# Kernel optimization log

Measured on AMD Instinct MI355X. Metric: run time of the kernel, lower is better.

Reference implementation:

```python
import jax, jax.numpy as jnp
import numpy as np

N = 50000
E = 800000
F0, F1, F2 = 256, 128, 64
EPS = 1e-5


def setup_inputs() -> dict:
    key = jax.random.key(0)
    ks = jax.random.split(key, 20)
    x = jax.random.normal(ks[0], (N, F0), dtype=jnp.float32)
    src = jax.random.randint(ks[1], (E,), 0, N)
    dst = jax.random.randint(ks[2], (E,), 0, N)
    edge_index = jnp.stack([src, dst]).astype(jnp.int64)

    def lin(k, fi, fo):
        s = 1.0 / np.sqrt(fi)
        k1, k2 = jax.random.split(k)
        W = jax.random.uniform(k1, (fi, fo), minval=-s, maxval=s, dtype=jnp.float32)
        b = jax.random.uniform(k2, (fo,), minval=-s, maxval=s, dtype=jnp.float32)
        return W, b

    We1, be1 = lin(ks[3], F0, F1)
    We2, be2 = lin(ks[4], F1, F2)
    Wd1, bd1 = lin(ks[5], F2, F1)
    Wd2, bd2 = lin(ks[6], F1, F0)
    return {
        'x': x, 'edge_index': edge_index,
        'We1': We1, 'be1': be1, 'g1': jnp.ones((F1,)), 'bb1': jnp.zeros((F1,)),
        'We2': We2, 'be2': be2, 'g2': jnp.ones((F2,)), 'bb2': jnp.zeros((F2,)),
        'Wd1': Wd1, 'bd1': bd1, 'g3': jnp.ones((F1,)), 'bb3': jnp.zeros((F1,)),
        'Wd2': Wd2, 'bd2': bd2, 'g4': jnp.ones((F0,)), 'bb4': jnp.zeros((F0,)),
    }


def _gcn(x, W, b, src, dst, dinv_src_dst, dinv_self):
    # PyG GCNConv: linear first, then sym-normalized propagation with self-loops
    h = x @ W + b                               # [N, Fout]
    msg = h[src] * dinv_src_dst[:, None]        # [E, Fout]
    out = jax.ops.segment_sum(msg, dst, num_segments=N)
    return out + h * dinv_self[:, None]         # self-loop term


def _bn(x, g, b):
    # BatchNorm1d training-mode: biased batch stats over node dim
    m = jnp.mean(x, axis=0)
    v = jnp.mean(jnp.square(x - m), axis=0)
    return g * (x - m) * jax.lax.rsqrt(v + EPS) + b


def reference(x, edge_index, We1, be1, g1, bb1, We2, be2, g2, bb2,
              Wd1, bd1, g3, bb3, Wd2, bd2, g4, bb4):
    src, dst = edge_index[0], edge_index[1]
    deg = jnp.zeros((N,), x.dtype).at[dst].add(1.0) + 1.0  # in-degree + self-loop
    dinv = jax.lax.rsqrt(deg)
    dsd = dinv[src] * dinv[dst]
    dself = dinv * dinv

    relu = jax.nn.relu
    # Encoder block 0 (outer i==0): relu(GCN), relu(BN)
    h = relu(_gcn(x, We1, be1, src, dst, dsd, dself))
    h = relu(_bn(h, g1, bb1))
    enc1 = h
    # Encoder block 1 (outer i==1 == len(inner)-1): relu(GCN), BN (no relu)
    h = relu(_gcn(h, We2, be2, src, dst, dsd, dself))
    h = _bn(h, g2, bb2)
    enc2 = h
    # Decoder block 0: relu(GCN), relu(BN)
    h = relu(_gcn(h, Wd1, bd1, src, dst, dsd, dself))
    h = relu(_bn(h, g3, bb3))
    # Decoder block 1 (i==1): relu(GCN), BN (no relu)
    h = relu(_gcn(h, Wd2, bd2, src, dst, dsd, dself))
    h = _bn(h, g4, bb4)
    # AE returns (reconstruction, encoded_embeddings)
    return h, enc1, enc2
```

## Files before the change

### kernel.cpp

```cpp
#include <hip/hip_runtime.h>
#include <hip/hip_fp16.h>

#define N_NODES 50000
#define F0 256
#define F1 128
#define F2 64
#define BN_EPS 1e-5f

typedef float f32x4 __attribute__((ext_vector_type(4)));
typedef __bf16 bf16x8 __attribute__((ext_vector_type(8)));
typedef unsigned short ushort8v __attribute__((ext_vector_type(8)));

__device__ __forceinline__ float bflo(unsigned v) { return __uint_as_float(v << 16); }
__device__ __forceinline__ float bfhi(unsigned v) { return __uint_as_float(v & 0xFFFF0000u); }
__device__ __forceinline__ unsigned short f2bf(float f) {
  unsigned u = __float_as_uint(f);
  u += 0x7FFFu + ((u >> 16) & 1u);
  return (unsigned short)(u >> 16);
}
__device__ __forceinline__ void split2(float a, unsigned short& hi, unsigned short& lo) {
  hi = f2bf(a);
  float hf = __uint_as_float((unsigned)hi << 16);
  lo = f2bf(a - hf);
}
__device__ __forceinline__ int rdl(int v, int l) { return __builtin_amdgcn_readlane(v, l); }
__device__ __forceinline__ float h2f(unsigned short h) {
  __half hh = *reinterpret_cast<__half*>(&h);
  return __half2float(hh);
}
__device__ __forceinline__ unsigned short f2h(float f) {
  __half hh = __float2half(f);
  return *reinterpret_cast<unsigned short*>(&hh);
}

__global__ void count_dst(const int* __restrict__ dst, int* __restrict__ counts,
                          int* __restrict__ eslot, int E) {
  int e = blockIdx.x * blockDim.x + threadIdx.x;
  if (e < E) eslot[e] = atomicAdd(&counts[dst[e]], 1);
}

__global__ __launch_bounds__(256) void scan_blocks(const int* __restrict__ counts,
                                                   int* __restrict__ offs,
                                                   int* __restrict__ bsum,
                                                   float* __restrict__ dinv) {
  __shared__ int s_w[4];
  const int tid = threadIdx.x, lane = tid & 63, wid = tid >> 6;
  const int base = blockIdx.x * 1024 + tid * 4;
  int v0 = 0, v1 = 0, v2 = 0, v3 = 0;
  if (base + 3 < N_NODES) {
    int4 v = *(const int4*)(counts + base);
    v0 = v.x; v1 = v.y; v2 = v.z; v3 = v.w;
  } else if (base < N_NODES) {
    v0 = counts[base];
    if (base + 1 < N_NODES) v1 = counts[base + 1];
    if (base + 2 < N_NODES) v2 = counts[base + 2];
  }
  if (base < N_NODES) {
    dinv[base] = rsqrtf((float)v0 + 1.0f);
    if (base + 1 < N_NODES) dinv[base + 1] = rsqrtf((float)v1 + 1.0f);
    if (base + 2 < N_NODES) dinv[base + 2] = rsqrtf((float)v2 + 1.0f);
    if (base + 3 < N_NODES) dinv[base + 3] = rsqrtf((float)v3 + 1.0f);
  }
  int t = v0 + v1 + v2 + v3;
  int incl = t;
#pragma unroll
  for (int d = 1; d < 64; d <<= 1) {
    int x = __shfl_up(incl, d);
    if (lane >= d) incl += x;
  }
  if (lane == 63) s_w[wid] = incl;
  __syncthreads();
  int woff = 0;
#pragma unroll
  for (int j = 0; j < 4; j++)
    if (j < wid) woff += s_w[j];
  int p = woff + incl - t;
  if (base < N_NODES) offs[base] = p;
  p += v0;
  if (base + 1 < N_NODES) offs[base + 1] = p;
  p += v1;
  if (base + 2 < N_NODES) offs[base + 2] = p;
  p += v2;
  if (base + 3 < N_NODES) offs[base + 3] = p;
  if (tid == 255) bsum[blockIdx.x] = woff + incl;
}

__global__ void scan_tops(int* __restrict__ bsum, int* __restrict__ offs, int nblk) {
  int lane = threadIdx.x;
  int v = (lane < nblk) ? bsum[lane] : 0;
  int incl = v;
#pragma unroll
  for (int d = 1; d < 64; d <<= 1) {
    int x = __shfl_up(incl, d);
    if (lane >= d) incl += x;
  }
  if (lane < nblk) bsum[lane] = incl - v;
  if (lane == 63) offs[N_NODES] = incl;
}

__global__ __launch_bounds__(256) void scan_add(int* __restrict__ offs,
                                                const int* __restrict__ bsum) {
  const int add = bsum[blockIdx.x];
  const int base = blockIdx.x * 1024 + threadIdx.x * 4;
  if (base + 3 < N_NODES) {
    int4 v = *(const int4*)(offs + base);
    v.x += add; v.y += add; v.z += add; v.w += add;
    *(int4*)(offs + base) = v;
  } else if (base < N_NODES) {
    offs[base] += add;
    if (base + 1 < N_NODES) offs[base + 1] += add;
    if (base + 2 < N_NODES) offs[base + 2] += add;
  }
}

__global__ void fill_csr(const int* __restrict__ src, const int* __restrict__ dst,
                         const int* __restrict__ offs, const int* __restrict__ eslot,
                         const float* __restrict__ dinv,
                         unsigned* __restrict__ csrU, int E) {
  int e = blockIdx.x * blockDim.x + threadIdx.x;
  if (e < E) {
    int s = src[e], d = dst[e];
    int p = offs[d] + eslot[e];
    unsigned ent = (unsigned)s | ((unsigned)f2h(dinv[s]) << 16);
    __builtin_nontemporal_store(ent, &csrU[p]);
  }
}

__global__ void compute_rowsum(const int* __restrict__ offs,
                               const unsigned* __restrict__ csrU,
                               const float* __restrict__ dinv, float* __restrict__ rowsum) {
  int i = blockIdx.x * blockDim.x + threadIdx.x;
  if (i < N_NODES) {
    float di = dinv[i];
    float s = di;
    int e1 = offs[i + 1];
    for (int e = offs[i]; e < e1; e++) s += h2f((unsigned short)(csrU[e] >> 16));
    rowsum[i] = di * s;
  }
}

__device__ __forceinline__ void wt_one(const float* W, unsigned short* Wh, unsigned short* Wl,
                                       int K, int N, int idx) {
  int k = idx / N, n = idx - k * N;
  unsigned short h, l;
  split2(W[idx], h, l);
  Wh[(size_t)n * K + k] = h;
  Wl[(size_t)n * K + k] = l;
}

__global__ void convert_weights(const float* __restrict__ We1, const float* __restrict__ We2,
                                const float* __restrict__ Wd1, const float* __restrict__ Wd2,
                                unsigned short* W1h, unsigned short* W1l,
                                unsigned short* W2h, unsigned short* W2l,
                                unsigned short* W3h, unsigned short* W3l,
                                unsigned short* W4h, unsigned short* W4l) {
  int idx = blockIdx.x * blockDim.x + threadIdx.x;
  if (idx < 32768) {
    wt_one(We1, W1h, W1l, 256, 128, idx);
  } else if (idx < 40960) {
    wt_one(We2, W2h, W2l, 128, 64, idx - 32768);
  } else if (idx < 49152) {
    wt_one(Wd1, W3h, W3l, 64, 128, idx - 40960);
  } else if (idx < 81920) {
    wt_one(Wd2, W4h, W4l, 128, 256, idx - 49152);
  }
}

template <int BN, bool STATS, bool AF32>
__global__ __launch_bounds__(256) void mfma_gemm_split(
    const unsigned short* __restrict__ Ahi, const unsigned short* __restrict__ Alo,
    const float* __restrict__ Af,
    const unsigned short* __restrict__ Whi, const unsigned short* __restrict__ Wlo,
    const float* __restrict__ bias, const float* __restrict__ rowsum,
    unsigned short* __restrict__ Cb, float* __restrict__ Cf,
    float* __restrict__ stat, int M, int K, int N) {
  constexpr int BM = 128;
  constexpr int MT = (BN == 128) ? 4 : 2;
  constexpr int NT = 4;
  __shared__ __align__(16) unsigned short AsH[4][BM][8];
  __shared__ __align__(16) unsigned short AsL[4][BM][8];
  __shared__ __align__(16) unsigned short BsH[4][BN][8];
  __shared__ __align__(16) unsigned short BsL[4][BN][8];
  const int tid = threadIdx.x;
  const int lane = tid & 63, wid = tid >> 6;
  const int quad = lane >> 4, ln = lane & 15;
  const int m0 = blockIdx.x * BM;
  const int n0 = blockIdx.y * BN;
  const int wm = (BN == 128) ? (wid & 1) * 64 : wid * 32;
  const int wn = (BN == 128) ? (wid >> 1) * 64 : 0;
  f32x4 acc[MT][NT] = {};

  const int arow = tid >> 2, aseg = tid & 3;
  for (int k0 = 0; k0 < K; k0 += 32) {
#pragma unroll
    for (int i = 0; i < 2; i++) {
      int row = arow + i * 64;
      int gm = m0 + row;
      if (AF32) {
        float4 u0 = make_float4(0.f, 0.f, 0.f, 0.f), u1 = u0;
        if (gm < M) {
          u0 = *(const float4*)(Af + (size_t)gm * K + k0 + aseg * 8);
          u1 = *(const float4*)(Af + (size_t)gm * K + k0 + aseg * 8 + 4);
        }
        ushort4 h0, l0, h1, l1;
        split2(u0.x, h0.x, l0.x); split2(u0.y, h0.y, l0.y);
        split2(u0.z, h0.z, l0.z); split2(u0.w, h0.w, l0.w);
        split2(u1.x, h1.x, l1.x); split2(u1.y, h1.y, l1.y);
        split2(u1.z, h1.z, l1.z); split2(u1.w, h1.w, l1.w);
        *(ushort4*)(&AsH[aseg][row][0]) = h0;
        *(ushort4*)(&AsH[aseg][row][4]) = h1;
        *(ushort4*)(&AsL[aseg][row][0]) = l0;
        *(ushort4*)(&AsL[aseg][row][4]) = l1;
      } else {
        ushort8v vh = {0, 0, 0, 0, 0, 0, 0, 0};
        ushort8v vl = {0, 0, 0, 0, 0, 0, 0, 0};
        if (gm < M) {
          vh = *(const ushort8v*)(Ahi + (size_t)gm * K + k0 + aseg * 8);
          vl = *(const ushort8v*)(Alo + (size_t)gm * K + k0 + aseg * 8);
        }
        *(ushort8v*)(&AsH[aseg][row][0]) = vh;
        *(ushort8v*)(&AsL[aseg][row][0]) = vl;
      }
    }
#pragma unroll
    for (int i = 0; i < BN / 64; i++) {
      int n = arow + i * 64;
      *(ushort8v*)(&BsH[aseg][n][0]) =
          *(const ushort8v*)(Whi + (size_t)(n0 + n) * K + k0 + aseg * 8);
      *(ushort8v*)(&BsL[aseg][n][0]) =
          *(const ushort8v*)(Wlo + (size_t)(n0 + n) * K + k0 + aseg * 8);
    }
    __syncthreads();
    bf16x8 ah[MT], al[MT], bh[NT], bl[NT];
#pragma unroll
    for (int mt = 0; mt < MT; mt++) {
      ah[mt] = *(const bf16x8*)(&AsH[quad][wm + mt * 16 + ln][0]);
      al[mt] = *(const bf16x8*)(&AsL[quad][wm + mt * 16 + ln][0]);
    }
#pragma unroll
    for (int nt = 0; nt < NT; nt++) {
      bh[nt] = *(const bf16x8*)(&BsH[quad][wn + nt * 16 + ln][0]);
      bl[nt] = *(const bf16x8*)(&BsL[quad][wn + nt * 16 + ln][0]);
    }
#pragma unroll
    for (int mt = 0; mt < MT; mt++)
#pragma unroll
      for (int nt = 0; nt < NT; nt++) {
        acc[mt][nt] = __builtin_amdgcn_mfma_f32_16x16x32_bf16(ah[mt], bl[nt], acc[mt][nt], 0, 0, 0);
        acc[mt][nt] = __builtin_amdgcn_mfma_f32_16x16x32_bf16(al[mt], bh[nt], acc[mt][nt], 0, 0, 0);
        acc[mt][nt] = __builtin_amdgcn_mfma_f32_16x16x32_bf16(ah[mt], bh[nt], acc[mt][nt], 0, 0, 0);
      }
    __syncthreads();
  }

  if (!STATS) {
#pragma unroll
    for (int nt = 0; nt < NT; nt++) {
      int gn = n0 + wn + nt * 16 + ln;
      float bv = bias[gn];
#pragma unroll
      for (int mt = 0; mt < MT; mt++) {
#pragma unroll
        for (int r = 0; r < 4; r++) {
          int gm = m0 + wm + mt * 16 + quad * 4 + r;
          if (gm < M) Cb[(size_t)gm * N + gn] = f2bf(acc[mt][nt][r] + bv);
        }
      }
    }
  } else {
    float rs[MT][4];
#pragma unroll
    for (int mt = 0; mt < MT; mt++)
#pragma unroll
      for (int r = 0; r < 4; r++) {
        int gm = m0 + wm + mt * 16 + quad * 4 + r;
        rs[mt][r] = (gm < M) ? rowsum[gm] : 0.f;
      }
#pragma unroll
    for (int nt = 0; nt < NT; nt++) {
      int gn = n0 + wn + nt * 16 + ln;
      float bv = bias[gn];
      float ls = 0.f, lq = 0.f;
#pragma unroll
      for (int mt = 0; mt < MT; mt++) {
#pragma unroll
        for (int r = 0; r < 4; r++) {
          int gm = m0 + wm + mt * 16 + quad * 4 + r;
          if (gm < M) {
            float v = fmaxf(fmaf(bv, rs[mt][r], acc[mt][nt][r]), 0.f);
            Cf[(size_t)gm * N + gn] = v;
            ls += v;
            lq = fmaf(v, v, lq);
          }
        }
      }
      ls += __shfl_xor(ls, 16); ls += __shfl_xor(ls, 32);
      lq += __shfl_xor(lq, 16); lq += __shfl_xor(lq, 32);
      if (quad == 0) {
        atomicAdd(&stat[gn], ls);
        atomicAdd(&stat[256 + gn], lq);
      }
    }
  }
}

template <bool RELU_STATS, bool OUT_SPLIT>
__global__ __launch_bounds__(256) void agg128_rl(
    const unsigned short* __restrict__ hb, const int* __restrict__ offs,
    const unsigned* __restrict__ csrU, const float* __restrict__ dinv,
    float* __restrict__ outf, unsigned short* __restrict__ outhi,
    unsigned short* __restrict__ outlo, float* __restrict__ stat) {
  const int tid = threadIdx.x;
  const int lane = tid & 63;
  const int widx = tid >> 6;
  const int nwaves = gridDim.x * 4;
  float ls0 = 0.f, ls1 = 0.f, lq0 = 0.f, lq1 = 0.f;

  for (int node = blockIdx.x * 4 + widx; node < N_NODES; node += nwaves) {
    const int e0 = __builtin_amdgcn_readfirstlane(offs[node]);
    const int e1 = __builtin_amdgcn_readfirstlane(offs[node + 1]);
    float a0 = 0.f, a1 = 0.f;
    for (int e = e0; e < e1; e += 64) {
      const int cnt = min(64, e1 - e);
      unsigned ent = 0;
      if (lane < cnt) ent = csrU[e + lane];
      const int nb = (cnt + 7) & ~7;
      for (int j = 0; j < nb; j += 8) {
#pragma unroll
        for (int u = 0; u < 8; u++) {
          unsigned ce = (unsigned)rdl((int)ent, j + u);
          int s = (int)(ce & 0xFFFFu);
          float w = h2f((unsigned short)(ce >> 16));
          unsigned v = *(const unsigned*)(hb + (size_t)s * 128 + lane * 2);
          a0 = fmaf(bflo(v), w, a0);
          a1 = fmaf(bfhi(v), w, a1);
        }
      }
    }
    float di = dinv[node];
    unsigned vs = *(const unsigned*)(hb + (size_t)node * 128 + lane * 2);
    a0 = fmaf(bflo(vs), di, a0) * di;
    a1 = fmaf(bfhi(vs), di, a1) * di;
    if (RELU_STATS) {
      a0 = fmaxf(a0, 0.f);
      a1 = fmaxf(a1, 0.f);
      ls0 += a0; ls1 += a1;
      lq0 = fmaf(a0, a0, lq0);
      lq1 = fmaf(a1, a1, lq1);
    }
    if (OUT_SPLIT) {
      unsigned short h0, l0, h1, l1;
      split2(a0, h0, l0);
      split2(a1, h1, l1);
      *(unsigned*)(outhi + (size_t)node * 128 + lane * 2) = (unsigned)h0 | ((unsigned)h1 << 16);
      *(unsigned*)(outlo + (size_t)node * 128 + lane * 2) = (unsigned)l0 | ((unsigned)l1 << 16);
    } else {
      *(float2*)(outf + (size_t)node * 128 + lane * 2) = make_float2(a0, a1);
    }
  }

  if (RELU_STATS) {
    __shared__ float red[4][128];
    red[widx][lane * 2 + 0] = ls0;
    red[widx][lane * 2 + 1] = ls1;
    __syncthreads();
    if (tid < 128) {
      atomicAdd(&stat[tid], red[0][tid] + red[1][tid] + red[2][tid] + red[3][tid]);
    }
    __syncthreads();
    red[widx][lane * 2 + 0] = lq0;
    red[widx][lane * 2 + 1] = lq1;
    __syncthreads();
    if (tid < 128) {
      atomicAdd(&stat[256 + tid], red[0][tid] + red[1][tid] + red[2][tid] + red[3][tid]);
    }
  }
}

template <bool RELU_STATS, bool OUT_SPLIT>
__global__ __launch_bounds__(256) void agg64_rl(
    const unsigned short* __restrict__ hb, const int* __restrict__ offs,
    const unsigned* __restrict__ csrU, const float* __restrict__ dinv,
    float* __restrict__ outf, unsigned short* __restrict__ outhi,
    unsigned short* __restrict__ outlo, float* __restrict__ stat) {
  const int tid = threadIdx.x;
  const int lane = tid & 63;
  const int widx = tid >> 6;
  const int half = lane >> 5;
  const int hl = lane & 31;
  const int nwaves = gridDim.x * 4;
  float ls0 = 0.f, ls1 = 0.f, lq0 = 0.f, lq1 = 0.f;

  for (int node = blockIdx.x * 4 + widx; node < N_NODES; node += nwaves) {
    const int e0 = __builtin_amdgcn_readfirstlane(offs[node]);
    const int e1 = __builtin_amdgcn_readfirstlane(offs[node + 1]);
    float a0 = 0.f, a1 = 0.f;
    for (int e = e0; e < e1; e += 64) {
      const int cnt = min(64, e1 - e);
      unsigned ent = 0;
      if (lane < cnt) ent = csrU[e + lane];
      const int nb = (cnt + 15) & ~15;
      for (int j = 0; j < nb; j += 16) {
#pragma unroll
        for (int u = 0; u < 8; u++) {
          unsigned ca = (unsigned)rdl((int)ent, j + 2 * u);
          unsigned cb = (unsigned)rdl((int)ent, j + 2 * u + 1);
          unsigned ce = half ? cb : ca;
          int s = (int)(ce & 0xFFFFu);
          float w = h2f((unsigned short)(ce >> 16));
          unsigned v = *(const unsigned*)(hb + (size_t)s * 64 + hl * 2);
          a0 = fmaf(bflo(v), w, a0);
          a1 = fmaf(bfhi(v), w, a1);
        }
      }
    }
    a0 += __shfl_xor(a0, 32);
    a1 += __shfl_xor(a1, 32);
    float di = dinv[node];
    unsigned vs = *(const unsigned*)(hb + (size_t)node * 64 + hl * 2);
    a0 = fmaf(bflo(vs), di, a0) * di;
    a1 = fmaf(bfhi(vs), di, a1) * di;
    if (RELU_STATS) {
      a0 = fmaxf(a0, 0.f);
      a1 = fmaxf(a1, 0.f);
      if (half == 0) {
        ls0 += a0; ls1 += a1;
        lq0 = fmaf(a0, a0, lq0);
        lq1 = fmaf(a1, a1, lq1);
      }
    }
    if (half == 0) {
      if (OUT_SPLIT) {
        unsigned short h0, l0, h1, l1;
        split2(a0, h0, l0);
        split2(a1, h1, l1);
        *(unsigned*)(outhi + (size_t)node * 64 + hl * 2) = (unsigned)h0 | ((unsigned)h1 << 16);
        *(unsigned*)(outlo + (size_t)node * 64 + hl * 2) = (unsigned)l0 | ((unsigned)l1 << 16);
      } else {
        *(float2*)(outf + (size_t)node * 64 + hl * 2) = make_float2(a0, a1);
      }
    }
  }

  if (RELU_STATS) {
    __shared__ float red[4][64];
    if (half == 0) {
      red[widx][hl * 2 + 0] = ls0;
      red[widx][hl * 2 + 1] = ls1;
    }
    __syncthreads();
    if (tid < 64) {
      atomicAdd(&stat[tid], red[0][tid] + red[1][tid] + red[2][tid] + red[3][tid]);
    }
    __syncthreads();
    if (half == 0) {
      red[widx][hl * 2 + 0] = lq0;
      red[widx][hl * 2 + 1] = lq1;
    }
    __syncthreads();
    if (tid < 64) {
      atomicAdd(&stat[256 + tid], red[0][tid] + red[1][tid] + red[2][tid] + red[3][tid]);
    }
  }
}

template <int F, bool RELU, bool WF32, bool WB16, bool WSPLIT>
__global__ __launch_bounds__(256) void bn_apply_f(const float* __restrict__ a,
                                                  const float* __restrict__ stat,
                                                  const float* __restrict__ g,
                                                  const float* __restrict__ bb,
                                                  float* __restrict__ outf,
                                                  unsigned short* __restrict__ outb,
                                                  unsigned short* __restrict__ outhi,
                                                  unsigned short* __restrict__ outlo) {
  __shared__ float s_scale[F], s_shift[F];
  const int tid = threadIdx.x;
  if (tid < F) {
    const float invN = 1.0f / (float)N_NODES;
    float mean = stat[tid] * invN;
    float var = fmaxf(stat[256 + tid] * invN - mean * mean, 0.f);
    float inv = rsqrtf(var + BN_EPS);
    float sc = g[tid] * inv;
    s_scale[tid] = sc;
    s_shift[tid] = bb[tid] - mean * sc;
  }
  __syncthreads();
  constexpr int C4 = F / 4;
  const int total = N_NODES * C4;
  for (int idx = blockIdx.x * blockDim.x + tid; idx < total; idx += gridDim.x * blockDim.x) {
    int c4 = idx % C4;
    float4 v = ((const float4*)a)[idx];
    float4 s = *(float4*)&s_scale[c4 * 4];
    float4 sh = *(float4*)&s_shift[c4 * 4];
    float4 o;
    o.x = fmaf(v.x, s.x, sh.x);
    o.y = fmaf(v.y, s.y, sh.y);
    o.z = fmaf(v.z, s.z, sh.z);
    o.w = fmaf(v.w, s.w, sh.w);
    if (RELU) {
      o.x = fmaxf(o.x, 0.f);
      o.y = fmaxf(o.y, 0.f);
      o.z = fmaxf(o.z, 0.f);
      o.w = fmaxf(o.w, 0.f);
    }
    if (WF32) ((float4*)outf)[idx] = o;
    if (WB16) {
      ushort4 b;
      b.x = f2bf(o.x); b.y = f2bf(o.y); b.z = f2bf(o.z); b.w = f2bf(o.w);
      ((ushort4*)outb)[idx] = b;
    }
    if (WSPLIT) {
      ushort4 h, l;
      split2(o.x, h.x, l.x);
      split2(o.y, h.y, l.y);
      split2(o.z, h.z, l.z);
      split2(o.w, h.w, l.w);
      ((ushort4*)outhi)[idx] = h;
      ((ushort4*)outlo)[idx] = l;
    }
  }
}

extern "C" void kernel_launch(void* const* d_in, const int* in_sizes, int n_in,
                              void* d_out, int out_size, void* d_ws, size_t ws_size,
                              hipStream_t stream) {
  const float* x = (const float*)d_in[0];
  const int* ei = (const int*)d_in[1];
  const int E = in_sizes[1] / 2;
  const int* src = ei;
  const int* dst = ei + E;
  const float* We1 = (const float*)d_in[2];  const float* be1 = (const float*)d_in[3];
  const float* g1  = (const float*)d_in[4];  const float* bb1 = (const float*)d_in[5];
  const float* We2 = (const float*)d_in[6];  const float* be2 = (const float*)d_in[7];
  const float* g2  = (const float*)d_in[8];  const float* bb2 = (const float*)d_in[9];
  const float* Wd1 = (const float*)d_in[10]; const float* bd1 = (const float*)d_in[11];
  const float* g3  = (const float*)d_in[12]; const float* bb3 = (const float*)d_in[13];
  const float* Wd2 = (const float*)d_in[14]; const float* bd2 = (const float*)d_in[15];
  const float* g4  = (const float*)d_in[16]; const float* bb4 = (const float*)d_in[17];

  float* out = (float*)d_out;
  char* ws = (char*)d_ws;
  unsigned short* A0b  = (unsigned short*)(ws + 0);
  unsigned short* A1b  = (unsigned short*)(ws + 12800000);
  unsigned short* C2b  = (unsigned short*)(ws + 32000000);
  unsigned short* G3hi = (unsigned short*)(ws + 0);
  unsigned short* G3lo = (unsigned short*)(ws + 6400000);
  unsigned short* D3b  = (unsigned short*)(ws + 12800000);
  unsigned short* G4hi = (unsigned short*)(ws + 0);
  unsigned short* G4lo = (unsigned short*)(ws + 25600000);
  unsigned short* Wb   = (unsigned short*)(ws + 48000000);
  unsigned short* W1h = Wb;            unsigned short* W1l = W1h + 32768;
  unsigned short* W2h = W1l + 32768;   unsigned short* W2l = W2h + 8192;
  unsigned short* W3h = W2l + 8192;    unsigned short* W3l = W3h + 8192;
  unsigned short* W4h = W3l + 8192;    unsigned short* W4l = W4h + 32768;
  float* B0f  = (float*)(ws + 51200000);
  int*   eslot  = (int*)(ws + 51200000);
  unsigned* csrU = (unsigned*)(ws + 102400000);
  float* stat4  = (float*)(ws + 108800000);
  int*   bsum   = (int*)(ws + 108808192);
  int*   counts = (int*)(ws + 108810000);
  int*   offs   = (int*)(ws + 109210000);
  float* dinv   = (float*)(ws + 109410064);
  if (ws_size < 109604160) return;
  float* rowsum = (float*)counts;

  float* enc1 = out + (size_t)N_NODES * F0;
  float* enc2 = enc1 + (size_t)N_NODES * F1;

  const int EB = (E + 255) / 256;
  const int AGG_GRID = 2048;
  const int MB = (N_NODES + 127) / 128;
  const int SCAN_B = (N_NODES + 1023) / 1024;

  convert_weights<<<320, 256, 0, stream>>>(We1, We2, Wd1, Wd2, W1h, W1l, W2h, W2l,
                                           W3h, W3l, W4h, W4l);
  hipMemsetAsync(counts, 0, N_NODES * sizeof(int), stream);
  hipMemsetAsync(stat4, 0, 4 * 512 * sizeof(float), stream);
  count_dst<<<EB, 256, 0, stream>>>(dst, counts, eslot, E);
  scan_blocks<<<SCAN_B, 256, 0, stream>>>(counts, offs, bsum, dinv);
  scan_tops<<<1, 64, 0, stream>>>(bsum, offs, SCAN_B);
  scan_add<<<SCAN_B, 256, 0, stream>>>(offs, bsum);
  fill_csr<<<EB, 256, 0, stream>>>(src, dst, offs, eslot, dinv, csrU, E);
  compute_rowsum<<<(N_NODES + 255) / 256, 256, 0, stream>>>(offs, csrU, dinv, rowsum);

  mfma_gemm_split<128, false, true><<<dim3(MB, 1), 256, 0, stream>>>(
      nullptr, nullptr, x, W1h, W1l, be1, nullptr, A0b, nullptr, nullptr, N_NODES, F0, F1);
  agg128_rl<true, false><<<AGG_GRID, 256, 0, stream>>>(
      A0b, offs, csrU, dinv, B0f, nullptr, nullptr, stat4);
  bn_apply_f<F1, true, true, false, false><<<2048, 256, 0, stream>>>(
      B0f, stat4, g1, bb1, enc1, nullptr, nullptr, nullptr);

  mfma_gemm_split<64, false, true><<<dim3(MB, 1), 256, 0, stream>>>(
      nullptr, nullptr, enc1, W2h, W2l, be2, nullptr, A1b, nullptr, nullptr, N_NODES, F1, F2);
  agg64_rl<true, false><<<AGG_GRID, 256, 0, stream>>>(
      A1b, offs, csrU, dinv, B0f, nullptr, nullptr, stat4 + 512);
  bn_apply_f<F2, false, true, true, false><<<2048, 256, 0, stream>>>(
      B0f, stat4 + 512, g2, bb2, enc2, C2b, nullptr, nullptr);

  agg64_rl<false, true><<<AGG_GRID, 256, 0, stream>>>(
      C2b, offs, csrU, dinv, nullptr, G3hi, G3lo, nullptr);
  mfma_gemm_split<128, true, false><<<dim3(MB, 1), 256, 0, stream>>>(
      G3hi, G3lo, nullptr, W3h, W3l, bd1, rowsum, nullptr, B0f, stat4 + 1024, N_NODES, F2, F1);
  bn_apply_f<F1, true, false, true, false><<<2048, 256, 0, stream>>>(
      B0f, stat4 + 1024, g3, bb3, nullptr, D3b, nullptr, nullptr);

  agg128_rl<false, true><<<AGG_GRID, 256, 0, stream>>>(
      D3b, offs, csrU, dinv, nullptr, G4hi, G4lo, nullptr);
  mfma_gemm_split<128, true, false><<<dim3(MB, 2), 256, 0, stream>>>(
      G4hi, G4lo, nullptr, W4h, W4l, bd2, rowsum, nullptr, B0f, stat4 + 1536, N_NODES, F1, F0);
  bn_apply_f<F0, false, true, false, false><<<2048, 256, 0, stream>>>(
      B0f, stat4 + 1536, g4, bb4, out, nullptr, nullptr, nullptr);
}
```

Baseline: 590.4 us.

## Split neighbor aggregation into two column-half passes with nontemporal CSR/output access

Each aggregation kernel now processes only half of the feature columns per launch, using two launches with a column offset. This shrinks the gathered working set per pass so more of the feature table can stay in cache during the random gathers. Each wave also spreads more edges across its lanes (2 or 4 edges in parallel). CSR loads and outputs use nontemporal hints to avoid polluting cache. In exchange the CSR index stream is read twice and each pass pays its own launch and reduction overhead.

```diff
diff --git a/kernel.cpp b/kernel.cpp
--- a/kernel.cpp
+++ b/kernel.cpp
@@ -304,16 +304,20 @@
   }
 }
 
+
 template <bool RELU_STATS, bool OUT_SPLIT>
-__global__ __launch_bounds__(256) void agg128_rl(
+__global__ __launch_bounds__(256) void agg128h(
     const unsigned short* __restrict__ hb, const int* __restrict__ offs,
     const unsigned* __restrict__ csrU, const float* __restrict__ dinv,
     float* __restrict__ outf, unsigned short* __restrict__ outhi,
-    unsigned short* __restrict__ outlo, float* __restrict__ stat) {
+    unsigned short* __restrict__ outlo, float* __restrict__ stat, int c0) {
   const int tid = threadIdx.x;
   const int lane = tid & 63;
   const int widx = tid >> 6;
+  const int half = lane >> 5;
+  const int hl = lane & 31;
   const int nwaves = gridDim.x * 4;
+  const unsigned short* hbc = hb + c0;
   float ls0 = 0.f, ls1 = 0.f, lq0 = 0.f, lq1 = 0.f;
 
   for (int node = blockIdx.x * 4 + widx; node < N_NODES; node += nwaves) {
@@ -323,82 +327,7 @@
     for (int e = e0; e < e1; e += 64) {
       const int cnt = min(64, e1 - e);
       unsigned ent = 0;
-      if (lane < cnt) ent = csrU[e + lane];
-      const int nb = (cnt + 7) & ~7;
-      for (int j = 0; j < nb; j += 8) {
-#pragma unroll
-        for (int u = 0; u < 8; u++) {
-          unsigned ce = (unsigned)rdl((int)ent, j + u);
-          int s = (int)(ce & 0xFFFFu);
-          float w = h2f((unsigned short)(ce >> 16));
-          unsigned v = *(const unsigned*)(hb + (size_t)s * 128 + lane * 2);
-          a0 = fmaf(bflo(v), w, a0);
-          a1 = fmaf(bfhi(v), w, a1);
-        }
-      }
-    }
-    float di = dinv[node];
-    unsigned vs = *(const unsigned*)(hb + (size_t)node * 128 + lane * 2);
-    a0 = fmaf(bflo(vs), di, a0) * di;
-    a1 = fmaf(bfhi(vs), di, a1) * di;
-    if (RELU_STATS) {
-      a0 = fmaxf(a0, 0.f);
-      a1 = fmaxf(a1, 0.f);
-      ls0 += a0; ls1 += a1;
-      lq0 = fmaf(a0, a0, lq0);
-      lq1 = fmaf(a1, a1, lq1);
-    }
-    if (OUT_SPLIT) {
-      unsigned short h0, l0, h1, l1;
-      split2(a0, h0, l0);
-      split2(a1, h1, l1);
-      *(unsigned*)(outhi + (size_t)node * 128 + lane * 2) = (unsigned)h0 | ((unsigned)h1 << 16);
-      *(unsigned*)(outlo + (size_t)node * 128 + lane * 2) = (unsigned)l0 | ((unsigned)l1 << 16);
-    } else {
-      *(float2*)(outf + (size_t)node * 128 + lane * 2) = make_float2(a0, a1);
-    }
-  }
-
-  if (RELU_STATS) {
-    __shared__ float red[4][128];
-    red[widx][lane * 2 + 0] = ls0;
-    red[widx][lane * 2 + 1] = ls1;
-    __syncthreads();
-    if (tid < 128) {
-      atomicAdd(&stat[tid], red[0][tid] + red[1][tid] + red[2][tid] + red[3][tid]);
-    }
-    __syncthreads();
-    red[widx][lane * 2 + 0] = lq0;
-    red[widx][lane * 2 + 1] = lq1;
-    __syncthreads();
-    if (tid < 128) {
-      atomicAdd(&stat[256 + tid], red[0][tid] + red[1][tid] + red[2][tid] + red[3][tid]);
-    }
-  }
-}
-
-template <bool RELU_STATS, bool OUT_SPLIT>
-__global__ __launch_bounds__(256) void agg64_rl(
-    const unsigned short* __restrict__ hb, const int* __restrict__ offs,
-    const unsigned* __restrict__ csrU, const float* __restrict__ dinv,
-    float* __restrict__ outf, unsigned short* __restrict__ outhi,
-    unsigned short* __restrict__ outlo, float* __restrict__ stat) {
-  const int tid = threadIdx.x;
-  const int lane = tid & 63;
-  const int widx = tid >> 6;
-  const int half = lane >> 5;
-  const int hl = lane & 31;
-  const int nwaves = gridDim.x * 4;
-  float ls0 = 0.f, ls1 = 0.f, lq0 = 0.f, lq1 = 0.f;
-
-  for (int node = blockIdx.x * 4 + widx; node < N_NODES; node += nwaves) {
-    const int e0 = __builtin_amdgcn_readfirstlane(offs[node]);
-    const int e1 = __builtin_amdgcn_readfirstlane(offs[node + 1]);
-    float a0 = 0.f, a1 = 0.f;
-    for (int e = e0; e < e1; e += 64) {
-      const int cnt = min(64, e1 - e);
-      unsigned ent = 0;
-      if (lane < cnt) ent = csrU[e + lane];
+      if (lane < cnt) ent = __builtin_nontemporal_load(&csrU[e + lane]);
       const int nb = (cnt + 15) & ~15;
       for (int j = 0; j < nb; j += 16) {
 #pragma unroll
@@ -408,7 +337,7 @@
           unsigned ce = half ? cb : ca;
           int s = (int)(ce & 0xFFFFu);
           float w = h2f((unsigned short)(ce >> 16));
-          unsigned v = *(const unsigned*)(hb + (size_t)s * 64 + hl * 2);
+          unsigned v = *(const unsigned*)(hbc + (size_t)s * 128 + hl * 2);
           a0 = fmaf(bflo(v), w, a0);
           a1 = fmaf(bfhi(v), w, a1);
         }
@@ -417,7 +346,7 @@
     a0 += __shfl_xor(a0, 32);
     a1 += __shfl_xor(a1, 32);
     float di = dinv[node];
-    unsigned vs = *(const unsigned*)(hb + (size_t)node * 64 + hl * 2);
+    unsigned vs = *(const unsigned*)(hbc + (size_t)node * 128 + hl * 2);
     a0 = fmaf(bflo(vs), di, a0) * di;
     a1 = fmaf(bfhi(vs), di, a1) * di;
     if (RELU_STATS) {
@@ -430,14 +359,16 @@
       }
     }
     if (half == 0) {
+      size_t p = (size_t)node * 128 + c0 + hl * 2;
       if (OUT_SPLIT) {
         unsigned short h0, l0, h1, l1;
         split2(a0, h0, l0);
         split2(a1, h1, l1);
-        *(unsigned*)(outhi + (size_t)node * 64 + hl * 2) = (unsigned)h0 | ((unsigned)h1 << 16);
-        *(unsigned*)(outlo + (size_t)node * 64 + hl * 2) = (unsigned)l0 | ((unsigned)l1 << 16);
+        __builtin_nontemporal_store((unsigned)h0 | ((unsigned)h1 << 16), (unsigned*)(outhi + p));
+        __builtin_nontemporal_store((unsigned)l0 | ((unsigned)l1 << 16), (unsigned*)(outlo + p));
       } else {
-        *(float2*)(outf + (size_t)node * 64 + hl * 2) = make_float2(a0, a1);
+        __builtin_nontemporal_store(a0, outf + p);
+        __builtin_nontemporal_store(a1, outf + p + 1);
       }
     }
   }
@@ -450,7 +381,7 @@
     }
     __syncthreads();
     if (tid < 64) {
-      atomicAdd(&stat[tid], red[0][tid] + red[1][tid] + red[2][tid] + red[3][tid]);
+      atomicAdd(&stat[c0 + tid], red[0][tid] + red[1][tid] + red[2][tid] + red[3][tid]);
     }
     __syncthreads();
     if (half == 0) {
@@ -459,7 +390,102 @@
     }
     __syncthreads();
     if (tid < 64) {
-      atomicAdd(&stat[256 + tid], red[0][tid] + red[1][tid] + red[2][tid] + red[3][tid]);
+      atomicAdd(&stat[256 + c0 + tid], red[0][tid] + red[1][tid] + red[2][tid] + red[3][tid]);
+    }
+  }
+}
+
+template <bool RELU_STATS, bool OUT_SPLIT>
+__global__ __launch_bounds__(256) void agg64h(
+    const unsigned short* __restrict__ hb, const int* __restrict__ offs,
+    const unsigned* __restrict__ csrU, const float* __restrict__ dinv,
+    float* __restrict__ outf, unsigned short* __restrict__ outhi,
+    unsigned short* __restrict__ outlo, float* __restrict__ stat, int c0) {
+  const int tid = threadIdx.x;
+  const int lane = tid & 63;
+  const int widx = tid >> 6;
+  const int q = lane >> 4;
+  const int ql = lane & 15;
+  const int nwaves = gridDim.x * 4;
+  const unsigned short* hbc = hb + c0;
+  float ls0 = 0.f, ls1 = 0.f, lq0 = 0.f, lq1 = 0.f;
+
+  for (int node = blockIdx.x * 4 + widx; node < N_NODES; node += nwaves) {
+    const int e0 = __builtin_amdgcn_readfirstlane(offs[node]);
+    const int e1 = __builtin_amdgcn_readfirstlane(offs[node + 1]);
+    float a0 = 0.f, a1 = 0.f;
+    for (int e = e0; e < e1; e += 64) {
+      const int cnt = min(64, e1 - e);
+      unsigned ent = 0;
+      if (lane < cnt) ent = __builtin_nontemporal_load(&csrU[e + lane]);
+      const int nb = (cnt + 7) & ~7;
+      for (int j = 0; j < nb; j += 8) {
+#pragma unroll
+        for (int u = 0; u < 2; u++) {
+          int b = j + 4 * u;
+          unsigned ea = (unsigned)rdl((int)ent, b + 0);
+          unsigned eb = (unsigned)rdl((int)ent, b + 1);
+          unsigned ec = (unsigned)rdl((int)ent, b + 2);
+          unsigned ed = (unsigned)rdl((int)ent, b + 3);
+          unsigned cx = (q & 1) ? eb : ea;
+          unsigned cy = (q & 1) ? ed : ec;
+          unsigned ce = (q & 2) ? cy : cx;
+          int s = (int)(ce & 0xFFFFu);
+          float w = h2f((unsigned short)(ce >> 16));
+          unsigned v = *(const unsigned*)(hbc + (size_t)s * 64 + ql * 2);
+          a0 = fmaf(bflo(v), w, a0);
+          a1 = fmaf(bfhi(v), w, a1);
+        }
+      }
+    }
+    a0 += __shfl_xor(a0, 16); a0 += __shfl_xor(a0, 32);
+    a1 += __shfl_xor(a1, 16); a1 += __shfl_xor(a1, 32);
+    float di = dinv[node];
+    unsigned vs = *(const unsigned*)(hbc + (size_t)node * 64 + ql * 2);
+    a0 = fmaf(bflo(vs), di, a0) * di;
+    a1 = fmaf(bfhi(vs), di, a1) * di;
+    if (RELU_STATS) {
+      a0 = fmaxf(a0, 0.f);
+      a1 = fmaxf(a1, 0.f);
+      if (q == 0) {
+        ls0 += a0; ls1 += a1;
+        lq0 = fmaf(a0, a0, lq0);
+        lq1 = fmaf(a1, a1, lq1);
+      }
+    }
+    if (q == 0) {
+      size_t p = (size_t)node * 64 + c0 + ql * 2;
+      if (OUT_SPLIT) {
+        unsigned short h0, l0, h1, l1;
+        split2(a0, h0, l0);
+        split2(a1, h1, l1);
+        __builtin_nontemporal_store((unsigned)h0 | ((unsigned)h1 << 16), (unsigned*)(outhi + p));
+        __builtin_nontemporal_store((unsigned)l0 | ((unsigned)l1 << 16), (unsigned*)(outlo + p));
+      } else {
+        __builtin_nontemporal_store(a0, outf + p);
+        __builtin_nontemporal_store(a1, outf + p + 1);
+      }
+    }
+  }
+
+  if (RELU_STATS) {
+    __shared__ float red[4][32];
+    if (q == 0) {
+      red[widx][ql * 2 + 0] = ls0;
+      red[widx][ql * 2 + 1] = ls1;
+    }
+    __syncthreads();
+    if (tid < 32) {
+      atomicAdd(&stat[c0 + tid], red[0][tid] + red[1][tid] + red[2][tid] + red[3][tid]);
+    }
+    __syncthreads();
+    if (q == 0) {
+      red[widx][ql * 2 + 0] = lq0;
+      red[widx][ql * 2 + 1] = lq1;
+    }
+    __syncthreads();
+    if (tid < 32) {
+      atomicAdd(&stat[256 + c0 + tid], red[0][tid] + red[1][tid] + red[2][tid] + red[3][tid]);
     }
   }
 }
@@ -585,27 +611,35 @@
 
   mfma_gemm_split<128, false, true><<<dim3(MB, 1), 256, 0, stream>>>(
       nullptr, nullptr, x, W1h, W1l, be1, nullptr, A0b, nullptr, nullptr, N_NODES, F0, F1);
-  agg128_rl<true, false><<<AGG_GRID, 256, 0, stream>>>(
-      A0b, offs, csrU, dinv, B0f, nullptr, nullptr, stat4);
+  agg128h<true, false><<<AGG_GRID, 256, 0, stream>>>(
+      A0b, offs, csrU, dinv, B0f, nullptr, nullptr, stat4, 0);
+  agg128h<true, false><<<AGG_GRID, 256, 0, stream>>>(
+      A0b, offs, csrU, dinv, B0f, nullptr, nullptr, stat4, 64);
   bn_apply_f<F1, true, true, false, false><<<2048, 256, 0, stream>>>(
       B0f, stat4, g1, bb1, enc1, nullptr, nullptr, nullptr);
 
   mfma_gemm_split<64, false, true><<<dim3(MB, 1), 256, 0, stream>>>(
       nullptr, nullptr, enc1, W2h, W2l, be2, nullptr, A1b, nullptr, nullptr, N_NODES, F1, F2);
-  agg64_rl<true, false><<<AGG_GRID, 256, 0, stream>>>(
-      A1b, offs, csrU, dinv, B0f, nullptr, nullptr, stat4 + 512);
+  agg64h<true, false><<<AGG_GRID, 256, 0, stream>>>(
+      A1b, offs, csrU, dinv, B0f, nullptr, nullptr, stat4 + 512, 0);
+  agg64h<true, false><<<AGG_GRID, 256, 0, stream>>>(
+      A1b, offs, csrU, dinv, B0f, nullptr, nullptr, stat4 + 512, 32);
   bn_apply_f<F2, false, true, true, false><<<2048, 256, 0, stream>>>(
       B0f, stat4 + 512, g2, bb2, enc2, C2b, nullptr, nullptr);
 
-  agg64_rl<false, true><<<AGG_GRID, 256, 0, stream>>>(
-      C2b, offs, csrU, dinv, nullptr, G3hi, G3lo, nullptr);
+  agg64h<false, true><<<AGG_GRID, 256, 0, stream>>>(
+      C2b, offs, csrU, dinv, nullptr, G3hi, G3lo, nullptr, 0);
+  agg64h<false, true><<<AGG_GRID, 256, 0, stream>>>(
+      C2b, offs, csrU, dinv, nullptr, G3hi, G3lo, nullptr, 32);
   mfma_gemm_split<128, true, false><<<dim3(MB, 1), 256, 0, stream>>>(
       G3hi, G3lo, nullptr, W3h, W3l, bd1, rowsum, nullptr, B0f, stat4 + 1024, N_NODES, F2, F1);
   bn_apply_f<F1, true, false, true, false><<<2048, 256, 0, stream>>>(
       B0f, stat4 + 1024, g3, bb3, nullptr, D3b, nullptr, nullptr);
 
-  agg128_rl<false, true><<<AGG_GRID, 256, 0, stream>>>(
-      D3b, offs, csrU, dinv, nullptr, G4hi, G4lo, nullptr);
+  agg128h<false, true><<<AGG_GRID, 256, 0, stream>>>(
+      D3b, offs, csrU, dinv, nullptr, G4hi, G4lo, nullptr, 0);
+  agg128h<false, true><<<AGG_GRID, 256, 0, stream>>>(
+      D3b, offs, csrU, dinv, nullptr, G4hi, G4lo, nullptr, 64);
   mfma_gemm_split<128, true, false><<<dim3(MB, 2), 256, 0, stream>>>(
       G4hi, G4lo, nullptr, W4h, W4l, bd2, rowsum, nullptr, B0f, stat4 + 1536, N_NODES, F1, F0);
   bn_apply_f<F0, false, true, false, false><<<2048, 256, 0, stream>>>(
```

Result: slower. 716.6 us (+21.4%).
